# Performance work log

Measured on AMD Instinct MI355X. Metric: run time of the kernel, lower is better.

## Reference

```python
import jax, jax.numpy as jnp
import numpy as np

B, N, C = 4, 3136, 64
IMG_H = IMG_W = 56
HEADS = 1
TOPK = 8
HID = 4 * C  # mlp_ratio=4.0


def _ln(x, g, b, eps=1e-5):
    m = x.mean(-1, keepdims=True)
    v = ((x - m) ** 2).mean(-1, keepdims=True)
    return (x - m) * jax.lax.rsqrt(v + eps) * g + b


def _conv(x, w, b, pad, groups):
    y = jax.lax.conv_general_dilated(
        x, w, (1, 1), [(pad, pad), (pad, pad)],
        dimension_numbers=('NCHW', 'OIHW', 'NCHW'), feature_group_count=groups)
    return y + b[None, :, None, None]


def setup_inputs() -> dict:
    key = jax.random.key(0)
    ks = jax.random.split(key, 10)
    def rn(k, shp, scale=0.02):
        return jax.random.normal(k, shp, jnp.float32) * scale
    return {
        'x': jax.random.normal(ks[0], (B, N, C), jnp.float32),
        'norm1_g': jnp.ones((C,), jnp.float32), 'norm1_b': jnp.zeros((C,), jnp.float32),
        'wq': rn(ks[1], (C, C)), 'bq': jnp.zeros((C,), jnp.float32),
        'wkv': rn(ks[2], (C, 2 * C)), 'bkv': jnp.zeros((2 * C,), jnp.float32),
        'wproj': rn(ks[3], (C, C)), 'bproj': jnp.zeros((C,), jnp.float32),
        'local_w': rn(ks[4], (C, C // HEADS, 3, 3), 0.05), 'local_b': jnp.zeros((C,), jnp.float32),
        'norm2_g': jnp.ones((C,), jnp.float32), 'norm2_b': jnp.zeros((C,), jnp.float32),
        'w3': rn(ks[5], (HID, 1, 3, 3), 0.05), 'b3': jnp.zeros((HID,), jnp.float32),
        'w5': rn(ks[6], (HID, 1, 5, 5), 0.05), 'b5': jnp.zeros((HID,), jnp.float32),
        'w1': rn(ks[7], (C, 2 * HID, 1, 1), 0.05), 'b1': jnp.zeros((C,), jnp.float32),
        'H': IMG_H, 'W': IMG_W,
    }


def reference(x, norm1_g, norm1_b, wq, bq, wkv, bkv, wproj, bproj,
              local_w, local_b, norm2_g, norm2_b, w3, b3, w5, b5, w1, b1, H, W):
    Bb, Nn, Cc = x.shape
    d = Cc // HEADS
    scale = d ** -0.5
    # --- DynamicSparseAttention (global branch) ---
    xn = _ln(x, norm1_g, norm1_b)
    q = (xn @ wq + bq).reshape(Bb, Nn, HEADS, d).transpose(0, 2, 1, 3)       # bhnd
    kv = (xn @ wkv + bkv).reshape(Bb, Nn, 2, HEADS, d)
    k = kv[:, :, 0].transpose(0, 2, 1, 3)
    v = kv[:, :, 1].transpose(0, 2, 1, 3)
    attn = jnp.einsum('bhnd,bhmd->bhnm', q, k) * scale                        # [B,h,N,N]
    kth = jax.lax.top_k(attn, TOPK)[0][..., -1:]                              # k-th largest per row
    mask = (attn >= kth).astype(attn.dtype)                                   # top-k scatter mask
    p = jax.nn.softmax(attn * mask, axis=-1)                                  # zeros kept (as in torch ref)
    g = jnp.einsum('bhnm,bhmd->bhnd', p, v).transpose(0, 2, 1, 3).reshape(Bb, Nn, Cc)
    g = g @ wproj + bproj
    # --- local conv attention branch ---
    x_img = x.transpose(0, 2, 1).reshape(Bb, Cc, H, W)
    loc = _conv(x_img, local_w, local_b, 1, HEADS).reshape(Bb, Cc, Nn).transpose(0, 2, 1)
    # --- residual 1 (note: norm1 params reused, as in source) ---
    x = x + _ln(g + loc, norm1_g, norm1_b)
    # --- MSFN ---
    xn2 = _ln(x, norm2_g, norm2_b).transpose(0, 2, 1).reshape(Bb, Cc, H, W)
    x3 = _conv(xn2, w3, b3, 1, Cc)   # depthwise 3x3, channel mult 4
    x5 = _conv(xn2, w5, b5, 2, Cc)   # depthwise 5x5, channel mult 4
    m = _conv(jnp.concatenate([x3, x5], axis=1), w1, b1, 0, 1)
    return x + m.reshape(Bb, Cc, Nn).transpose(0, 2, 1)
```

## Files before the change

kernel.cpp:

```cpp
#include <hip/hip_runtime.h>
#include <math.h>

#define Bv 4
#define Nv 3136
#define Cv 64
#define Hh 56
#define Ww 56
#define HIDv 256
#define TOPKv 8
#define TSP 520
#define LCP 584
#define XNP 72

constexpr float SCALE = 0.125f;
constexpr float EPS = 1e-5f;

typedef short bf16x8 __attribute__((ext_vector_type(8)));
typedef float f32x4 __attribute__((ext_vector_type(4)));

#define CSWAP(a, b) { unsigned int _hi = max(a, b); unsigned int _lo = min(a, b); a = _hi; b = _lo; }
#define BITONIC8(T) \
  CSWAP(T[0], T[4]); CSWAP(T[1], T[5]); CSWAP(T[2], T[6]); CSWAP(T[3], T[7]); \
  CSWAP(T[0], T[2]); CSWAP(T[1], T[3]); CSWAP(T[4], T[6]); CSWAP(T[5], T[7]); \
  CSWAP(T[0], T[1]); CSWAP(T[2], T[3]); CSWAP(T[4], T[5]); CSWAP(T[6], T[7]);

__device__ __forceinline__ unsigned short f2bf(float f) {
  unsigned int u = __float_as_uint(f);
  u = (u + 0x7FFFu + ((u >> 16) & 1u)) >> 16;
  return (unsigned short)u;
}
__device__ __forceinline__ float bf2f(unsigned short u) {
  return __uint_as_float(((unsigned int)u) << 16);
}
__device__ __forceinline__ unsigned int pack2(float a, float b) {
  return (unsigned int)f2bf(a) | ((unsigned int)f2bf(b) << 16);
}

__device__ __forceinline__ unsigned int packScore(float s, int j) {
  unsigned int b = __float_as_uint(s);
  unsigned int m = b ^ ((b & 0x80000000u) ? 0xFFFFFFFFu : 0x80000000u);
  return (m & 0xFFFFF000u) | (unsigned int)j;
}
__device__ __forceinline__ float unpackScore(unsigned int p) {
  unsigned int m = p & 0xFFFFF000u;
  unsigned int b = (m & 0x80000000u) ? (m ^ 0x80000000u) : ~m;
  return __uint_as_float(b);
}

__global__ void k_transpose(const float* __restrict__ w1, const float* __restrict__ lw,
                            const float* __restrict__ w3, const float* __restrict__ w5,
                            const float* __restrict__ wq, const float* __restrict__ wkv,
                            const float* __restrict__ bq, const float* __restrict__ bkv,
                            const float* __restrict__ wproj,
                            unsigned short* __restrict__ w1bf, unsigned short* __restrict__ lwb,
                            float* __restrict__ w3t, float* __restrict__ w5t,
                            unsigned short* __restrict__ wqkvt, float* __restrict__ qkvb,
                            unsigned short* __restrict__ wprojt) {
  int p = blockIdx.x * 256 + threadIdx.x;
  if (p < 64 * 512) w1bf[p] = f2bf(w1[p]);
  if (p < 64 * 576) {
    int co = p / 576, k = p % 576;
    int tap = k >> 6, ci = k & 63;
    lwb[p] = f2bf(lw[co * 576 + ci * 9 + tap]);
  }
  if (p < 36 * 64) {
    int cin = p & 63, tm = p >> 6;
    int tap = tm >> 2, m = tm & 3;
    w3t[p] = w3[(cin * 4 + m) * 9 + tap];
  }
  if (p < 100 * 64) {
    int cin = p & 63, tm = p >> 6;
    int tap = tm >> 2, m = tm & 3;
    w5t[p] = w5[(cin * 4 + m) * 25 + tap];
  }
  if (p < 192 * 64) {
    int o = p >> 6, i = p & 63;
    float v = (o < 64) ? wq[i * 64 + o] : wkv[i * 128 + (o - 64)];
    wqkvt[p] = f2bf(v);
  }
  if (p < 192) qkvb[p] = (p < 64) ? bq[p] : bkv[p - 64];
  if (p < 64 * 64) {
    int o = p >> 6, i = p & 63;
    wprojt[p] = f2bf(wproj[i * 64 + o]);
  }
}

__global__ __launch_bounds__(256) void k_ln_qkv(
    const float* __restrict__ x, const float* __restrict__ g1, const float* __restrict__ b1,
    const unsigned short* __restrict__ wqkvt, const float* __restrict__ qkvb,
    unsigned short* __restrict__ q16, unsigned short* __restrict__ k16,
    float* __restrict__ vo, float* __restrict__ sumv) {
  __shared__ __align__(16) unsigned short xnS[16 * XNP];
  int bid = blockIdx.x;
  int b = bid / 196, tile = bid % 196;
  size_t tok0 = (size_t)b * Nv + tile * 16;
  int t = threadIdx.x;
  int w = t >> 6, l = t & 63;
  int tokL = t >> 4;
  int ch0 = (t & 15) * 4;
  size_t tok = tok0 + tokL;
  float v[4];
  *(float4*)v = *(const float4*)&x[tok * 64 + ch0];
  float s = v[0] + v[1] + v[2] + v[3];
  float s2 = v[0] * v[0] + v[1] * v[1] + v[2] * v[2] + v[3] * v[3];
#pragma unroll
  for (int off = 1; off <= 8; off <<= 1) {
    s += __shfl_xor(s, off, 64);
    s2 += __shfl_xor(s2, off, 64);
  }
  float m = s * (1.f / 64.f);
  float rs = rsqrtf(s2 * (1.f / 64.f) - m * m + EPS);
  {
    unsigned int pk[2];
    float a0_ = (v[0] - m) * rs * g1[ch0] + b1[ch0];
    float a1_ = (v[1] - m) * rs * g1[ch0 + 1] + b1[ch0 + 1];
    float a2_ = (v[2] - m) * rs * g1[ch0 + 2] + b1[ch0 + 2];
    float a3_ = (v[3] - m) * rs * g1[ch0 + 3] + b1[ch0 + 3];
    pk[0] = pack2(a0_, a1_);
    pk[1] = pack2(a2_, a3_);
    *(uint2*)&xnS[tokL * XNP + ch0] = *(uint2*)pk;
  }
  __syncthreads();
  int n = l & 15, q = l >> 4;
  const bf16x8 a0 = *(const bf16x8*)&xnS[n * XNP + q * 8];
  const bf16x8 a1 = *(const bf16x8*)&xnS[n * XNP + 32 + q * 8];
  {
    const unsigned short* wr = &wqkvt[(size_t)(w * 16 + n) * 64];
    bf16x8 b0 = *(const bf16x8*)&wr[q * 8];
    bf16x8 b1_ = *(const bf16x8*)&wr[32 + q * 8];
    f32x4 acc = {0.f, 0.f, 0.f, 0.f};
    acc = __builtin_amdgcn_mfma_f32_16x16x32_bf16(a0, b0, acc, 0, 0, 0);
    acc = __builtin_amdgcn_mfma_f32_16x16x32_bf16(a1, b1_, acc, 0, 0, 0);
    float bias = qkvb[w * 16 + n];
#pragma unroll
    for (int r = 0; r < 4; ++r)
      q16[(tok0 + q * 4 + r) * 64 + w * 16 + n] = f2bf(acc[r] + bias);
  }
  {
    const unsigned short* wr = &wqkvt[(size_t)((w + 4) * 16 + n) * 64];
    bf16x8 b0 = *(const bf16x8*)&wr[q * 8];
    bf16x8 b1_ = *(const bf16x8*)&wr[32 + q * 8];
    f32x4 acc = {0.f, 0.f, 0.f, 0.f};
    acc = __builtin_amdgcn_mfma_f32_16x16x32_bf16(a0, b0, acc, 0, 0, 0);
    acc = __builtin_amdgcn_mfma_f32_16x16x32_bf16(a1, b1_, acc, 0, 0, 0);
    float bias = qkvb[64 + w * 16 + n];
#pragma unroll
    for (int r = 0; r < 4; ++r)
      k16[(tok0 + q * 4 + r) * 64 + w * 16 + n] = f2bf(acc[r] + bias);
  }
  {
    const unsigned short* wr = &wqkvt[(size_t)((w + 8) * 16 + n) * 64];
    bf16x8 b0 = *(const bf16x8*)&wr[q * 8];
    bf16x8 b1_ = *(const bf16x8*)&wr[32 + q * 8];
    f32x4 acc = {0.f, 0.f, 0.f, 0.f};
    acc = __builtin_amdgcn_mfma_f32_16x16x32_bf16(a0, b0, acc, 0, 0, 0);
    acc = __builtin_amdgcn_mfma_f32_16x16x32_bf16(a1, b1_, acc, 0, 0, 0);
    float bias = qkvb[128 + w * 16 + n];
    float vp = acc[0] + acc[1] + acc[2] + acc[3] + 4.0f * bias;
#pragma unroll
    for (int r = 0; r < 4; ++r)
      vo[(tok0 + q * 4 + r) * 64 + w * 16 + n] = acc[r] + bias;
    vp += __shfl_xor(vp, 16, 64);
    vp += __shfl_xor(vp, 32, 64);
    if (q == 0) atomicAdd(&sumv[b * 64 + w * 16 + n], vp);
  }
}

__global__ __launch_bounds__(256) void k_attn_topk(
    const unsigned short* __restrict__ q16, const unsigned short* __restrict__ k16,
    unsigned int* __restrict__ top8out) {
  __shared__ unsigned int candLDS[16][4][9];
  int bid = blockIdx.x;
  int quarter = bid & 3;
  int lin = bid >> 2;
  int b = lin / 196, tile = lin % 196;
  int qbase = b * Nv + tile * 16;
  size_t bN = (size_t)b * Nv;
  int t = threadIdx.x;
  int w = t >> 6, lane = t & 63;
  int qcol = lane & 15, quad = lane >> 4;

  const bf16x8 qf0 = *(const bf16x8*)&q16[((size_t)(qbase + qcol)) * 64 + quad * 8];
  const bf16x8 qf1 = *(const bf16x8*)&q16[((size_t)(qbase + qcol)) * 64 + 32 + quad * 8];

  unsigned int t8a[8], t8b[8];
  unsigned int PACKNEG = packScore(-1e30f, 0);
#pragma unroll
  for (int u = 0; u < 8; ++u) { t8a[u] = PACKNEG; t8b[u] = PACKNEG; }

  int chBeg = (quarter * 49) >> 2;
  int chEnd = ((quarter + 1) * 49) >> 2;
  int nch = chEnd - chBeg;
  int keyRow = w * 16 + qcol;
  const unsigned short* kbase = &k16[(bN + (size_t)chBeg * 64 + keyRow) * 64];

  bf16x8 ka0 = *(const bf16x8*)&kbase[quad * 8];
  bf16x8 ka1 = *(const bf16x8*)&kbase[32 + quad * 8];
  bf16x8 kb0 = *(const bf16x8*)&kbase[(size_t)64 * 64 + quad * 8];
  bf16x8 kb1 = *(const bf16x8*)&kbase[(size_t)64 * 64 + 32 + quad * 8];

#pragma unroll 1
  for (int i = 0; i + 1 < nch; i += 2) {
    bf16x8 ca0 = ka0, ca1 = ka1, cb0 = kb0, cb1 = kb1;
    int ia = min(i + 2, nch - 1), ib = min(i + 3, nch - 1);
    ka0 = *(const bf16x8*)&kbase[(size_t)ia * 4096 + quad * 8];
    ka1 = *(const bf16x8*)&kbase[(size_t)ia * 4096 + 32 + quad * 8];
    kb0 = *(const bf16x8*)&kbase[(size_t)ib * 4096 + quad * 8];
    kb1 = *(const bf16x8*)&kbase[(size_t)ib * 4096 + 32 + quad * 8];

    f32x4 accA = {0.f, 0.f, 0.f, 0.f};
    accA = __builtin_amdgcn_mfma_f32_16x16x32_bf16(ca0, qf0, accA, 0, 0, 0);
    accA = __builtin_amdgcn_mfma_f32_16x16x32_bf16(ca1, qf1, accA, 0, 0, 0);
    f32x4 accB = {0.f, 0.f, 0.f, 0.f};
    accB = __builtin_amdgcn_mfma_f32_16x16x32_bf16(cb0, qf0, accB, 0, 0, 0);
    accB = __builtin_amdgcn_mfma_f32_16x16x32_bf16(cb1, qf1, accB, 0, 0, 0);

    {
      int jb = (chBeg + i) * 64 + w * 16 + quad * 4;
      unsigned int p0 = packScore(accA[0], jb + 0);
      unsigned int p1 = packScore(accA[1], jb + 1);
      unsigned int p2 = packScore(accA[2], jb + 2);
      unsigned int p3 = packScore(accA[3], jb + 3);
      CSWAP(p0, p1); CSWAP(p2, p3); CSWAP(p0, p2); CSWAP(p1, p3); CSWAP(p1, p2);
      t8a[4] = max(t8a[4], p3);
      t8a[5] = max(t8a[5], p2);
      t8a[6] = max(t8a[6], p1);
      t8a[7] = max(t8a[7], p0);
      BITONIC8(t8a);
    }
    {
      int jb = (chBeg + i + 1) * 64 + w * 16 + quad * 4;
      unsigned int p0 = packScore(accB[0], jb + 0);
      unsigned int p1 = packScore(accB[1], jb + 1);
      unsigned int p2 = packScore(accB[2], jb + 2);
      unsigned int p3 = packScore(accB[3], jb + 3);
      CSWAP(p0, p1); CSWAP(p2, p3); CSWAP(p0, p2); CSWAP(p1, p3); CSWAP(p1, p2);
      t8b[4] = max(t8b[4], p3);
      t8b[5] = max(t8b[5], p2);
      t8b[6] = max(t8b[6], p1);
      t8b[7] = max(t8b[7], p0);
      BITONIC8(t8b);
    }
  }
  if (nch & 1) {
    f32x4 accA = {0.f, 0.f, 0.f, 0.f};
    accA = __builtin_amdgcn_mfma_f32_16x16x32_bf16(ka0, qf0, accA, 0, 0, 0);
    accA = __builtin_amdgcn_mfma_f32_16x16x32_bf16(ka1, qf1, accA, 0, 0, 0);
    int jb = (chEnd - 1) * 64 + w * 16 + quad * 4;
    unsigned int p0 = packScore(accA[0], jb + 0);
    unsigned int p1 = packScore(accA[1], jb + 1);
    unsigned int p2 = packScore(accA[2], jb + 2);
    unsigned int p3 = packScore(accA[3], jb + 3);
    CSWAP(p0, p1); CSWAP(p2, p3); CSWAP(p0, p2); CSWAP(p1, p3); CSWAP(p1, p2);
    t8a[4] = max(t8a[4], p3);
    t8a[5] = max(t8a[5], p2);
    t8a[6] = max(t8a[6], p1);
    t8a[7] = max(t8a[7], p0);
    BITONIC8(t8a);
  }

  unsigned int t8[8];
#pragma unroll
  for (int i = 0; i < 8; ++i) t8[i] = max(t8a[i], t8b[7 - i]);
  BITONIC8(t8);

#pragma unroll
  for (int step = 16; step <= 32; step <<= 1) {
    unsigned int o[8];
#pragma unroll
    for (int i = 0; i < 8; ++i) o[i] = (unsigned int)__shfl_xor((int)t8[i], step, 64);
    unsigned int nw[8];
#pragma unroll
    for (int i = 0; i < 8; ++i) nw[i] = max(t8[i], o[7 - i]);
#pragma unroll
    for (int i = 0; i < 8; ++i) t8[i] = nw[i];
    BITONIC8(t8);
  }
  if (quad == 0) {
#pragma unroll
    for (int i = 0; i < 8; ++i) candLDS[qcol][w][i] = t8[i];
  }
  __syncthreads();

  if (t < 16) {
    int r = t;
    int p0 = 0, p1 = 0, p2 = 0, p3 = 0;
    size_t obase = ((size_t)(bN + tile * 16 + r)) * 32 + quarter * 8;
#pragma unroll
    for (int u = 0; u < 8; ++u) {
      unsigned int c0 = (p0 < 8) ? candLDS[r][0][p0] : 0u;
      unsigned int c1 = (p1 < 8) ? candLDS[r][1][p1] : 0u;
      unsigned int c2 = (p2 < 8) ? candLDS[r][2][p2] : 0u;
      unsigned int c3 = (p3 < 8) ? candLDS[r][3][p3] : 0u;
      unsigned int best = c0;
      int bw = 0;
      if (c1 > best) { best = c1; bw = 1; }
      if (c2 > best) { best = c2; bw = 2; }
      if (c3 > best) { best = c3; bw = 3; }
      p0 += (bw == 0); p1 += (bw == 1); p2 += (bw == 2); p3 += (bw == 3);
      top8out[obase + u] = best;
    }
  }
}

__global__ __launch_bounds__(256) void k_attn_proj(
    const unsigned int* __restrict__ top8, const float* __restrict__ vg,
    const float* __restrict__ sumv, const float* __restrict__ x,
    const unsigned short* __restrict__ lwb, const float* __restrict__ lb,
    const unsigned short* __restrict__ wprojt, const float* __restrict__ bproj,
    const float* __restrict__ g1, const float* __restrict__ b1,
    const float* __restrict__ g2, const float* __restrict__ b2,
    float* __restrict__ x2, unsigned short* __restrict__ xn2b) {
  __shared__ float kwS[16][8];
  __shared__ int kidxS[16][8];
  __shared__ float invZS[16];
  __shared__ __align__(16) unsigned short imS[16 * LCP];
  __shared__ __align__(16) unsigned short gS[16 * XNP];
  __shared__ float yS[16 * 66];
  int bid = blockIdx.x;
  int b = bid / 196, rem = bid % 196;
  int th = rem / 7, tw = rem % 7;
  int h0 = th * 2, w0 = tw * 8;
  size_t bN = (size_t)b * Nv;
  int t = threadIdx.x;

  for (int p = t; p < 1152; p += 256) {
    int sub = p & 7, s = p >> 3;
    int tok = s / 9, tap = s % 9;
    int tr = tok >> 3, tc = tok & 7;
    int dh = tap / 3, dw = tap % 3;
    int gh = h0 + tr - 1 + dh, gw = w0 + tc - 1 + dw;
    uint4 uu = {0u, 0u, 0u, 0u};
    if (gh >= 0 && gh < Hh && gw >= 0 && gw < Ww) {
      const float* xp = &x[(bN + gh * Ww + gw) * 64 + sub * 8];
      float4 va = *(const float4*)xp;
      float4 vb = *(const float4*)(xp + 4);
      uu.x = pack2(va.x, va.y);
      uu.y = pack2(va.z, va.w);
      uu.z = pack2(vb.x, vb.y);
      uu.w = pack2(vb.z, vb.w);
    }
    *(uint4*)&imS[tok * LCP + tap * 64 + sub * 8] = uu;
  }

  if (t < 16) {
    int gtok = (h0 + (t >> 3)) * Ww + w0 + (t & 7);
    size_t base = (bN + gtok) * 32;
    unsigned int A[8];
#pragma unroll
    for (int i = 0; i < 8; ++i) A[i] = top8[base + i];
#pragma unroll
    for (int h = 1; h < 4; ++h) {
      unsigned int Bb[8];
#pragma unroll
      for (int i = 0; i < 8; ++i) Bb[i] = top8[base + h * 8 + i];
#pragma unroll
      for (int i = 0; i < 8; ++i) A[i] = max(A[i], Bb[7 - i]);
      BITONIC8(A);
    }
    float Z = (float)(Nv - TOPKv);
#pragma unroll
    for (int u = 0; u < 8; ++u) {
      float s = unpackScore(A[u]) * SCALE;
      float e = __expf(s);
      kwS[t][u] = e - 1.0f;
      kidxS[t][u] = (int)(A[u] & 0xFFFu);
      Z += e;
    }
    invZS[t] = 1.0f / Z;
  }
  __syncthreads();

  int w = t >> 6, l = t & 63;
  int n = l & 15, q = l >> 4;

  f32x4 lacc = {0.f, 0.f, 0.f, 0.f};
  {
    const unsigned short* lwrow = &lwb[(size_t)(w * 16 + n) * 576];
#pragma unroll 6
    for (int kk = 0; kk < 18; ++kk) {
      bf16x8 af = *(const bf16x8*)&imS[n * LCP + kk * 32 + q * 8];
      bf16x8 bfr = *(const bf16x8*)&lwrow[kk * 32 + q * 8];
      lacc = __builtin_amdgcn_mfma_f32_16x16x32_bf16(af, bfr, lacc, 0, 0, 0);
    }
  }
  float lbias = lb[w * 16 + n];

  {
    int c = t & 63, rg = t >> 6;
    float sv = sumv[b * 64 + c];
#pragma unroll
    for (int rr = 0; rr < 4; ++rr) {
      int tokL = rg * 4 + rr;
      float acc = sv;
#pragma unroll
      for (int u = 0; u < 8; ++u)
        acc += kwS[tokL][u] * vg[(bN + kidxS[tokL][u]) * 64 + c];
      gS[tokL * XNP + c] = f2bf(acc * invZS[tokL]);
    }
  }
  __syncthreads();

  {
    const bf16x8 a0 = *(const bf16x8*)&gS[n * XNP + q * 8];
    const bf16x8 a1 = *(const bf16x8*)&gS[n * XNP + 32 + q * 8];
    const unsigned short* wr = &wprojt[(size_t)(w * 16 + n) * 64];
    bf16x8 b0 = *(const bf16x8*)&wr[q * 8];
    bf16x8 b1_ = *(const bf16x8*)&wr[32 + q * 8];
    f32x4 acc = {0.f, 0.f, 0.f, 0.f};
    acc = __builtin_amdgcn_mfma_f32_16x16x32_bf16(a0, b0, acc, 0, 0, 0);
    acc = __builtin_amdgcn_mfma_f32_16x16x32_bf16(a1, b1_, acc, 0, 0, 0);
    float bias = bproj[w * 16 + n];
#pragma unroll
    for (int r = 0; r < 4; ++r)
      yS[(q * 4 + r) * 66 + w * 16 + n] = acc[r] + bias + lacc[r] + lbias;
  }
  __syncthreads();

  int tokL = t >> 4;
  int ch0 = (t & 15) * 4;
  size_t tok = bN + (size_t)(h0 + (tokL >> 3)) * Ww + w0 + (tokL & 7);
  float y[4];
#pragma unroll
  for (int i = 0; i < 4; ++i) y[i] = yS[tokL * 66 + ch0 + i];
  float s = y[0] + y[1] + y[2] + y[3];
  float s2 = y[0] * y[0] + y[1] * y[1] + y[2] * y[2] + y[3] * y[3];
#pragma unroll
  for (int off = 1; off <= 8; off <<= 1) {
    s += __shfl_xor(s, off, 64);
    s2 += __shfl_xor(s2, off, 64);
  }
  float m1 = s * (1.f / 64.f);
  float rs1 = rsqrtf(s2 * (1.f / 64.f) - m1 * m1 + EPS);
  float xv[4];
  *(float4*)xv = *(const float4*)&x[tok * 64 + ch0];
  float x2v[4];
  float t_s = 0.f, t_s2 = 0.f;
#pragma unroll
  for (int i = 0; i < 4; ++i) {
    float t1 = (y[i] - m1) * rs1 * g1[ch0 + i] + b1[ch0 + i];
    x2v[i] = xv[i] + t1;
    t_s += x2v[i];
    t_s2 += x2v[i] * x2v[i];
  }
#pragma unroll
  for (int off = 1; off <= 8; off <<= 1) {
    t_s += __shfl_xor(t_s, off, 64);
    t_s2 += __shfl_xor(t_s2, off, 64);
  }
  float m2 = t_s * (1.f / 64.f);
  float rs2 = rsqrtf(t_s2 * (1.f / 64.f) - m2 * m2 + EPS);
  *(float4*)&x2[tok * 64 + ch0] = *(float4*)x2v;
  unsigned int pk[2];
  {
    float a0_ = (x2v[0] - m2) * rs2 * g2[ch0] + b2[ch0];
    float a1_ = (x2v[1] - m2) * rs2 * g2[ch0 + 1] + b2[ch0 + 1];
    float a2_ = (x2v[2] - m2) * rs2 * g2[ch0 + 2] + b2[ch0 + 2];
    float a3_ = (x2v[3] - m2) * rs2 * g2[ch0 + 3] + b2[ch0 + 3];
    pk[0] = pack2(a0_, a1_);
    pk[1] = pack2(a2_, a3_);
  }
  *(uint2*)&xn2b[tok * 64 + ch0] = *(uint2*)pk;
}

__global__ __launch_bounds__(256) void k_msfn(
    const unsigned short* __restrict__ xn2b, const float* __restrict__ x2,
    const float* __restrict__ w3t, const float* __restrict__ b3,
    const float* __restrict__ w5t, const float* __restrict__ b5,
    const unsigned short* __restrict__ w1bf, const float* __restrict__ b1,
    float* __restrict__ out) {
  __shared__ __align__(16) unsigned short xtS[6 * 12 * 64];
  __shared__ __align__(16) unsigned short tsS[16 * TSP];

  int bid = blockIdx.x;
  int b = bid / 196;
  int rem = bid % 196;
  int th = rem / 7, tw = rem % 7;
  int h0 = th * 2, w0 = tw * 8;
  size_t bN = (size_t)b * Nv;
  int t = threadIdx.x;

  unsigned int* xtU = (unsigned int*)xtS;
  for (int p = t; p < 6 * 12 * 32; p += 256) {
    int cp = p & 31, rc = p >> 5;
    int r = rc / 12, cc = rc % 12;
    int gh = h0 - 2 + r, gw = w0 - 2 + cc;
    unsigned int v = 0;
    if (gh >= 0 && gh < Hh && gw >= 0 && gw < Ww)
      v = *(const unsigned int*)&xn2b[(bN + gh * Ww + gw) * 64 + cp * 2];
    xtU[rc * 32 + cp] = v;
  }
  __syncthreads();

  int cin = t & 63, tg = t >> 6;
  int tr = tg >> 1, tc0 = (tg & 1) * 4;
  float win[5][8];
#pragma unroll
  for (int r = 0; r < 5; ++r)
#pragma unroll
    for (int c = 0; c < 8; ++c)
      win[r][c] = bf2f(xtS[((tr + r) * 12 + tc0 + c) * 64 + cin]);

  unsigned int* tsU = (unsigned int*)tsS;
#pragma unroll 1
  for (int m2 = 0; m2 < 4; m2 += 2) {
    float a3[2][9], a5[2][25], bb3[2], bb5[2];
#pragma unroll
    for (int mm = 0; mm < 2; ++mm) {
      int m = m2 + mm;
#pragma unroll
      for (int tap = 0; tap < 9; ++tap) a3[mm][tap] = w3t[(tap * 4 + m) * 64 + cin];
#pragma unroll
      for (int tap = 0; tap < 25; ++tap) a5[mm][tap] = w5t[(tap * 4 + m) * 64 + cin];
      bb3[mm] = b3[cin * 4 + m];
      bb5[mm] = b5[cin * 4 + m];
    }
#pragma unroll
    for (int tk = 0; tk < 4; ++tk) {
      int tok = tg * 4 + tk;
      unsigned int p3 = 0, p5 = 0;
#pragma unroll
      for (int mm = 0; mm < 2; ++mm) {
        float acc3 = bb3[mm];
#pragma unroll
        for (int kh = 0; kh < 3; ++kh)
#pragma unroll
          for (int kw2 = 0; kw2 < 3; ++kw2)
            acc3 += win[1 + kh][tk + 1 + kw2] * a3[mm][kh * 3 + kw2];
        float acc5 = bb5[mm];
#pragma unroll
        for (int kh = 0; kh < 5; ++kh)
#pragma unroll
          for (int kw2 = 0; kw2 < 5; ++kw2)
            acc5 += win[kh][tk + kw2] * a5[mm][kh * 5 + kw2];
        p3 |= (unsigned int)f2bf(acc3) << (16 * mm);
        p5 |= (unsigned int)f2bf(acc5) << (16 * mm);
      }
      tsU[(tok * TSP + cin * 4 + m2) >> 1] = p3;
      tsU[(tok * TSP + 256 + cin * 4 + m2) >> 1] = p5;
    }
  }
  __syncthreads();

  int wv = tg, lane = t & 63;
  int n16 = lane & 15, quad = lane >> 4;
  const unsigned short* wrow = &w1bf[(size_t)(wv * 16 + n16) * 512];
  f32x4 acc = {0.f, 0.f, 0.f, 0.f};
#pragma unroll 4
  for (int kk = 0; kk < 16; ++kk) {
    bf16x8 af = *(const bf16x8*)&tsS[n16 * TSP + kk * 32 + quad * 8];
    bf16x8 bfr = *(const bf16x8*)&wrow[kk * 32 + quad * 8];
    acc = __builtin_amdgcn_mfma_f32_16x16x32_bf16(af, bfr, acc, 0, 0, 0);
  }
  float bias = b1[wv * 16 + n16];
#pragma unroll
  for (int r = 0; r < 4; ++r) {
    int tok = quad * 4 + r;
    int trr = tok >> 3, tcc = tok & 7;
    size_t idx = (bN + (size_t)(h0 + trr) * Ww + w0 + tcc) * 64 + wv * 16 + n16;
    out[idx] = x2[idx] + acc[r] + bias;
  }
}

extern "C" void kernel_launch(void* const* d_in, const int* in_sizes, int n_in,
                              void* d_out, int out_size, void* d_ws, size_t ws_size,
                              hipStream_t stream) {
  const float* x = (const float*)d_in[0];
  const float* n1g = (const float*)d_in[1];
  const float* n1b = (const float*)d_in[2];
  const float* wq = (const float*)d_in[3];
  const float* bq = (const float*)d_in[4];
  const float* wkv = (const float*)d_in[5];
  const float* bkv = (const float*)d_in[6];
  const float* wproj = (const float*)d_in[7];
  const float* bproj = (const float*)d_in[8];
  const float* lw = (const float*)d_in[9];
  const float* lb = (const float*)d_in[10];
  const float* n2g = (const float*)d_in[11];
  const float* n2b = (const float*)d_in[12];
  const float* w3 = (const float*)d_in[13];
  const float* b3 = (const float*)d_in[14];
  const float* w5 = (const float*)d_in[15];
  const float* b5 = (const float*)d_in[16];
  const float* w1 = (const float*)d_in[17];
  const float* b1 = (const float*)d_in[18];
  float* out = (float*)d_out;

  float* ws = (float*)d_ws;
  const size_t TOK = (size_t)Bv * Nv * Cv;
  float* vb = ws;
  float* sumv = vb + TOK;
  float* x2 = sumv + 256;
  float* w3t = x2 + TOK;
  float* w5t = w3t + 2304;
  float* qkvb = w5t + 6400;
  unsigned short* q16 = (unsigned short*)(qkvb + 192);
  unsigned short* k16 = q16 + TOK;
  unsigned short* xn2b = k16 + TOK;
  unsigned short* w1bf = xn2b + TOK;
  unsigned short* lwb = w1bf + 64 * 512;
  unsigned short* wqkvt = lwb + 64 * 576;
  unsigned short* wprojt = wqkvt + 192 * 64;
  unsigned int* top8ws = (unsigned int*)(wprojt + 64 * 64 + 64);

  hipMemsetAsync(sumv, 0, 256 * sizeof(float), stream);
  k_transpose<<<144, 256, 0, stream>>>(w1, lw, w3, w5, wq, wkv, bq, bkv, wproj,
                                       w1bf, lwb, w3t, w5t, wqkvt, qkvb, wprojt);
  k_ln_qkv<<<Bv * 196, 256, 0, stream>>>(x, n1g, n1b, wqkvt, qkvb, q16, k16, vb, sumv);
  k_attn_topk<<<Bv * 196 * 4, 256, 0, stream>>>(q16, k16, top8ws);
  k_attn_proj<<<Bv * 196, 256, 0, stream>>>(top8ws, vb, sumv, x, lwb, lb, wprojt, bproj,
                                            n1g, n1b, n2g, n2b, x2, xn2b);
  k_msfn<<<Bv * 196, 256, 0, stream>>>(xn2b, x2, w3t, b3, w5t, b5, w1bf, b1, out);
}
```

Baseline: 192.8 us.

## Split top-k key range into 8 per-wave partitions and drop LDS merge

The attention top-k kernel now uses 128-thread blocks where each wave owns a contiguous 392-key slice, giving 8 splits per query tile. Each wave keeps a single running top-8 list and writes it directly to global memory, which removes the shared-memory candidate merge and __syncthreads. The downstream projection kernel merges 8 partial lists instead of 4. The sumv zeroing moves from a separate memset into the weight-transpose kernel. In exchange there is a longer serial loop per wave with no two-chunk interleave, more partial-list traffic, and more merge work later.

```diff
diff --git a/kernel.cpp b/kernel.cpp
--- a/kernel.cpp
+++ b/kernel.cpp
@@ -11,6 +11,8 @@
 #define TSP 520
 #define LCP 584
 #define XNP 72
+#define KSPL 8
+#define KPS 392
 
 constexpr float SCALE = 0.125f;
 constexpr float EPS = 1e-5f;
@@ -55,8 +57,9 @@
                             unsigned short* __restrict__ w1bf, unsigned short* __restrict__ lwb,
                             float* __restrict__ w3t, float* __restrict__ w5t,
                             unsigned short* __restrict__ wqkvt, float* __restrict__ qkvb,
-                            unsigned short* __restrict__ wprojt) {
+                            unsigned short* __restrict__ wprojt, float* __restrict__ sumv) {
   int p = blockIdx.x * 256 + threadIdx.x;
+  if (p < 256) sumv[p] = 0.0f;
   if (p < 64 * 512) w1bf[p] = f2bf(w1[p]);
   if (p < 64 * 576) {
     int co = p / 576, k = p % 576;
@@ -166,103 +169,58 @@
   }
 }
 
-__global__ __launch_bounds__(256) void k_attn_topk(
+__global__ __launch_bounds__(128) void k_attn_topk(
     const unsigned short* __restrict__ q16, const unsigned short* __restrict__ k16,
     unsigned int* __restrict__ top8out) {
-  __shared__ unsigned int candLDS[16][4][9];
   int bid = blockIdx.x;
-  int quarter = bid & 3;
+  int w = threadIdx.x >> 6;
+  int lane = threadIdx.x & 63;
+  int split = ((bid & 3) << 1) | w;
   int lin = bid >> 2;
   int b = lin / 196, tile = lin % 196;
   int qbase = b * Nv + tile * 16;
   size_t bN = (size_t)b * Nv;
-  int t = threadIdx.x;
-  int w = t >> 6, lane = t & 63;
   int qcol = lane & 15, quad = lane >> 4;
 
   const bf16x8 qf0 = *(const bf16x8*)&q16[((size_t)(qbase + qcol)) * 64 + quad * 8];
   const bf16x8 qf1 = *(const bf16x8*)&q16[((size_t)(qbase + qcol)) * 64 + 32 + quad * 8];
 
-  unsigned int t8a[8], t8b[8];
+  unsigned int t8[8];
   unsigned int PACKNEG = packScore(-1e30f, 0);
 #pragma unroll
-  for (int u = 0; u < 8; ++u) { t8a[u] = PACKNEG; t8b[u] = PACKNEG; }
-
-  int chBeg = (quarter * 49) >> 2;
-  int chEnd = ((quarter + 1) * 49) >> 2;
-  int nch = chEnd - chBeg;
-  int keyRow = w * 16 + qcol;
-  const unsigned short* kbase = &k16[(bN + (size_t)chBeg * 64 + keyRow) * 64];
-
-  bf16x8 ka0 = *(const bf16x8*)&kbase[quad * 8];
-  bf16x8 ka1 = *(const bf16x8*)&kbase[32 + quad * 8];
-  bf16x8 kb0 = *(const bf16x8*)&kbase[(size_t)64 * 64 + quad * 8];
-  bf16x8 kb1 = *(const bf16x8*)&kbase[(size_t)64 * 64 + 32 + quad * 8];
+  for (int u = 0; u < 8; ++u) t8[u] = PACKNEG;
+
+  int kbase = split * KPS;
+  int m = lane & 15;
+  const int NCH = 25;
+
+  int row0 = min(kbase + m, Nv - 1);
+  bf16x8 kf0 = *(const bf16x8*)&k16[(bN + row0) * 64 + quad * 8];
+  bf16x8 kf1 = *(const bf16x8*)&k16[(bN + row0) * 64 + 32 + quad * 8];
 
 #pragma unroll 1
-  for (int i = 0; i + 1 < nch; i += 2) {
-    bf16x8 ca0 = ka0, ca1 = ka1, cb0 = kb0, cb1 = kb1;
-    int ia = min(i + 2, nch - 1), ib = min(i + 3, nch - 1);
-    ka0 = *(const bf16x8*)&kbase[(size_t)ia * 4096 + quad * 8];
-    ka1 = *(const bf16x8*)&kbase[(size_t)ia * 4096 + 32 + quad * 8];
-    kb0 = *(const bf16x8*)&kbase[(size_t)ib * 4096 + quad * 8];
-    kb1 = *(const bf16x8*)&kbase[(size_t)ib * 4096 + 32 + quad * 8];
-
-    f32x4 accA = {0.f, 0.f, 0.f, 0.f};
-    accA = __builtin_amdgcn_mfma_f32_16x16x32_bf16(ca0, qf0, accA, 0, 0, 0);
-    accA = __builtin_amdgcn_mfma_f32_16x16x32_bf16(ca1, qf1, accA, 0, 0, 0);
-    f32x4 accB = {0.f, 0.f, 0.f, 0.f};
-    accB = __builtin_amdgcn_mfma_f32_16x16x32_bf16(cb0, qf0, accB, 0, 0, 0);
-    accB = __builtin_amdgcn_mfma_f32_16x16x32_bf16(cb1, qf1, accB, 0, 0, 0);
-
-    {
-      int jb = (chBeg + i) * 64 + w * 16 + quad * 4;
-      unsigned int p0 = packScore(accA[0], jb + 0);
-      unsigned int p1 = packScore(accA[1], jb + 1);
-      unsigned int p2 = packScore(accA[2], jb + 2);
-      unsigned int p3 = packScore(accA[3], jb + 3);
-      CSWAP(p0, p1); CSWAP(p2, p3); CSWAP(p0, p2); CSWAP(p1, p3); CSWAP(p1, p2);
-      t8a[4] = max(t8a[4], p3);
-      t8a[5] = max(t8a[5], p2);
-      t8a[6] = max(t8a[6], p1);
-      t8a[7] = max(t8a[7], p0);
-      BITONIC8(t8a);
-    }
-    {
-      int jb = (chBeg + i + 1) * 64 + w * 16 + quad * 4;
-      unsigned int p0 = packScore(accB[0], jb + 0);
-      unsigned int p1 = packScore(accB[1], jb + 1);
-      unsigned int p2 = packScore(accB[2], jb + 2);
-      unsigned int p3 = packScore(accB[3], jb + 3);
-      CSWAP(p0, p1); CSWAP(p2, p3); CSWAP(p0, p2); CSWAP(p1, p3); CSWAP(p1, p2);
-      t8b[4] = max(t8b[4], p3);
-      t8b[5] = max(t8b[5], p2);
-      t8b[6] = max(t8b[6], p1);
-      t8b[7] = max(t8b[7], p0);
-      BITONIC8(t8b);
-    }
-  }
-  if (nch & 1) {
-    f32x4 accA = {0.f, 0.f, 0.f, 0.f};
-    accA = __builtin_amdgcn_mfma_f32_16x16x32_bf16(ka0, qf0, accA, 0, 0, 0);
-    accA = __builtin_amdgcn_mfma_f32_16x16x32_bf16(ka1, qf1, accA, 0, 0, 0);
-    int jb = (chEnd - 1) * 64 + w * 16 + quad * 4;
-    unsigned int p0 = packScore(accA[0], jb + 0);
-    unsigned int p1 = packScore(accA[1], jb + 1);
-    unsigned int p2 = packScore(accA[2], jb + 2);
-    unsigned int p3 = packScore(accA[3], jb + 3);
+  for (int ch = 0; ch < NCH; ++ch) {
+    bf16x8 c0 = kf0, c1 = kf1;
+    int nrow = min(kbase + min(ch + 1, NCH - 1) * 16 + m, Nv - 1);
+    kf0 = *(const bf16x8*)&k16[(bN + nrow) * 64 + quad * 8];
+    kf1 = *(const bf16x8*)&k16[(bN + nrow) * 64 + 32 + quad * 8];
+
+    f32x4 acc = {0.f, 0.f, 0.f, 0.f};
+    acc = __builtin_amdgcn_mfma_f32_16x16x32_bf16(c0, qf0, acc, 0, 0, 0);
+    acc = __builtin_amdgcn_mfma_f32_16x16x32_bf16(c1, qf1, acc, 0, 0, 0);
+
+    int jl = ch * 16 + quad * 4;
+    unsigned int p0 = (jl + 0 < KPS) ? packScore(acc[0], kbase + jl + 0) : 0u;
+    unsigned int p1 = (jl + 1 < KPS) ? packScore(acc[1], kbase + jl + 1) : 0u;
+    unsigned int p2 = (jl + 2 < KPS) ? packScore(acc[2], kbase + jl + 2) : 0u;
+    unsigned int p3 = (jl + 3 < KPS) ? packScore(acc[3], kbase + jl + 3) : 0u;
     CSWAP(p0, p1); CSWAP(p2, p3); CSWAP(p0, p2); CSWAP(p1, p3); CSWAP(p1, p2);
-    t8a[4] = max(t8a[4], p3);
-    t8a[5] = max(t8a[5], p2);
-    t8a[6] = max(t8a[6], p1);
-    t8a[7] = max(t8a[7], p0);
-    BITONIC8(t8a);
-  }
-
-  unsigned int t8[8];
-#pragma unroll
-  for (int i = 0; i < 8; ++i) t8[i] = max(t8a[i], t8b[7 - i]);
-  BITONIC8(t8);
+    t8[4] = max(t8[4], p3);
+    t8[5] = max(t8[5], p2);
+    t8[6] = max(t8[6], p1);
+    t8[7] = max(t8[7], p0);
+    BITONIC8(t8);
+  }
 
 #pragma unroll
   for (int step = 16; step <= 32; step <<= 1) {
@@ -277,29 +235,9 @@
     BITONIC8(t8);
   }
   if (quad == 0) {
-#pragma unroll
-    for (int i = 0; i < 8; ++i) candLDS[qcol][w][i] = t8[i];
-  }
-  __syncthreads();
-
-  if (t < 16) {
-    int r = t;
-    int p0 = 0, p1 = 0, p2 = 0, p3 = 0;
-    size_t obase = ((size_t)(bN + tile * 16 + r)) * 32 + quarter * 8;
-#pragma unroll
-    for (int u = 0; u < 8; ++u) {
-      unsigned int c0 = (p0 < 8) ? candLDS[r][0][p0] : 0u;
-      unsigned int c1 = (p1 < 8) ? candLDS[r][1][p1] : 0u;
-      unsigned int c2 = (p2 < 8) ? candLDS[r][2][p2] : 0u;
-      unsigned int c3 = (p3 < 8) ? candLDS[r][3][p3] : 0u;
-      unsigned int best = c0;
-      int bw = 0;
-      if (c1 > best) { best = c1; bw = 1; }
-      if (c2 > best) { best = c2; bw = 2; }
-      if (c3 > best) { best = c3; bw = 3; }
-      p0 += (bw == 0); p1 += (bw == 1); p2 += (bw == 2); p3 += (bw == 3);
-      top8out[obase + u] = best;
-    }
+    size_t obase = ((size_t)(bN + tile * 16 + qcol)) * 64 + split * 8;
+    *(uint4*)&top8out[obase] = make_uint4(t8[0], t8[1], t8[2], t8[3]);
+    *(uint4*)&top8out[obase + 4] = make_uint4(t8[4], t8[5], t8[6], t8[7]);
   }
 }
 
@@ -345,12 +283,12 @@
 
   if (t < 16) {
     int gtok = (h0 + (t >> 3)) * Ww + w0 + (t & 7);
-    size_t base = (bN + gtok) * 32;
+    size_t base = (bN + gtok) * 64;
     unsigned int A[8];
 #pragma unroll
     for (int i = 0; i < 8; ++i) A[i] = top8[base + i];
 #pragma unroll
-    for (int h = 1; h < 4; ++h) {
+    for (int h = 1; h < 8; ++h) {
       unsigned int Bb[8];
 #pragma unroll
       for (int i = 0; i < 8; ++i) Bb[i] = top8[base + h * 8 + i];
@@ -603,11 +541,10 @@
   unsigned short* wprojt = wqkvt + 192 * 64;
   unsigned int* top8ws = (unsigned int*)(wprojt + 64 * 64 + 64);
 
-  hipMemsetAsync(sumv, 0, 256 * sizeof(float), stream);
   k_transpose<<<144, 256, 0, stream>>>(w1, lw, w3, w5, wq, wkv, bq, bkv, wproj,
-                                       w1bf, lwb, w3t, w5t, wqkvt, qkvb, wprojt);
+                                       w1bf, lwb, w3t, w5t, wqkvt, qkvb, wprojt, sumv);
   k_ln_qkv<<<Bv * 196, 256, 0, stream>>>(x, n1g, n1b, wqkvt, qkvb, q16, k16, vb, sumv);
-  k_attn_topk<<<Bv * 196 * 4, 256, 0, stream>>>(q16, k16, top8ws);
+  k_attn_topk<<<Bv * 196 * 4, 128, 0, stream>>>(q16, k16, top8ws);
   k_attn_proj<<<Bv * 196, 256, 0, stream>>>(top8ws, vb, sumv, x, lwb, lb, wprojt, bproj,
                                             n1g, n1b, n2g, n2b, x2, xn2b);
   k_msfn<<<Bv * 196, 256, 0, stream>>>(xn2b, x2, w3t, b3, w5t, b5, w1bf, b1, out);
```

Measured after the change: 186.5 us. 3.3% less time.
